# Kernel optimization log

Measured on AMD Instinct MI355X. Metric: run time of the kernel, lower is better.

## Reference

```python
import jax, jax.numpy as jnp
import numpy as np

N_E = 4096      # n_embed
E_DIM = 64      # embed_dim
BETA = 0.25
DECAY = 0.99
EPS = 1e-05


def setup_inputs() -> dict:
    key = jax.random.key(0)
    k1, k2, k3, k4 = jax.random.split(key, 4)
    z = jax.random.normal(k1, (4, 64, 16, 32, 32), dtype=jnp.float32)
    # codebook initialized uniform(-1/n_e, 1/n_e) as in the torch module
    embed_w = jax.random.uniform(k2, (N_E, E_DIM), dtype=jnp.float32,
                                 minval=-1.0 / N_E, maxval=1.0 / N_E)
    cluster_size = jax.random.uniform(k3, (N_E,), dtype=jnp.float32)
    embed_avg = jax.random.normal(k4, (N_E, E_DIM), dtype=jnp.float32) * 0.01
    return {"z": z, "embed_w": embed_w, "cluster_size": cluster_size,
            "embed_avg": embed_avg}


def reference(z, embed_w, cluster_size, embed_avg):
    sg = jax.lax.stop_gradient
    # b c d h w -> b d h w c
    zp = jnp.transpose(z, (0, 2, 3, 4, 1))
    zf = zp.reshape(-1, E_DIM)                      # [N, e_dim]
    n_tok = zf.shape[0]
    # squared L2 distances to every code: [N, n_e]
    d = ((zf * zf).sum(axis=1, keepdims=True)
         + (embed_w * embed_w).sum(axis=1)
         - 2.0 * jnp.einsum('bd,nd->bn', zf, embed_w))
    idx = jnp.argmin(d, axis=1)                     # [N]
    z_q = embed_w[idx].reshape(zp.shape)            # codebook gather
    # perplexity from code-usage histogram (== mean of one-hot encodings)
    counts = jnp.zeros((N_E,), zf.dtype).at[idx].add(1.0)
    avg_probs = counts / n_tok
    perplexity = jnp.exp(-jnp.sum(avg_probs * jnp.log(avg_probs + 1e-10)))
    # EMA buffer updates (training mode; pure buffer math, no gradient flow)
    embed_sum = jnp.zeros((N_E, E_DIM), zf.dtype).at[idx].add(sg(zf))  # one_hot.T @ zf
    new_cs = cluster_size * DECAY + (1.0 - DECAY) * counts
    new_ea = embed_avg * DECAY + (1.0 - DECAY) * embed_sum
    n = new_cs.sum()
    smoothed_cs = (new_cs + EPS) / (n + N_E * EPS) * n
    new_embed = new_ea / smoothed_cs[:, None]
    # commitment loss and straight-through estimator
    loss = BETA * jnp.mean((sg(z_q) - zp) ** 2)
    z_q_st = zp + sg(z_q - zp)
    out = jnp.transpose(z_q_st, (0, 4, 1, 2, 3))    # b d h w c -> b c d h w
    return (out, loss, perplexity, idx, new_embed, new_cs, new_ea)
```

## Files before the change

### kernel.cpp

```cpp
#include <hip/hip_runtime.h>

static constexpr int NE   = 4096;
static constexpr int ED   = 64;
static constexpr int NTOK = 65536;
static constexpr int NCHUNK = 8;
static constexpr int CPC  = NE / NCHUNK;

static constexpr long O_OUT  = 0;
static constexpr long O_LOSS = 4194304;
static constexpr long O_PERP = 4194305;
static constexpr long O_IDX  = 4194306;
static constexpr long O_NEMB = 4259842;
static constexpr long O_NCS  = 4521986;
static constexpr long O_NEA  = 4526082;

static constexpr size_t W_ACC   = 0;
static constexpr size_t W_CNT   = 32;
static constexpr size_t W_CUR   = 16416;
static constexpr size_t W_OFF   = 32800;
static constexpr size_t W_BSQ   = 49184;
static constexpr size_t W_IDX   = 65568;
static constexpr size_t W_BKT   = 327712;
static constexpr size_t W_LOSSP = 589856;
static constexpr size_t W_PKD   = 720928;
static constexpr size_t W_ZERO_BYTES = 32800;
static constexpr size_t W_PKD_BYTES  = 524288;

__global__ __launch_bounds__(256) void kBsq(const float* __restrict__ e,
                                            float* __restrict__ bsq) {
    int n = blockIdx.x * 256 + threadIdx.x;
    const float* er = e + (n << 6);
    float a0 = 0.f, a1 = 0.f, a2 = 0.f, a3 = 0.f;
#pragma unroll
    for (int k = 0; k < ED; k += 4) {
        a0 = fmaf(er[k+0], er[k+0], a0);
        a1 = fmaf(er[k+1], er[k+1], a1);
        a2 = fmaf(er[k+2], er[k+2], a2);
        a3 = fmaf(er[k+3], er[k+3], a3);
    }
    bsq[n] = (a0 + a1) + (a2 + a3);
}

__global__ __launch_bounds__(256, 2) void kArgmin(const float* __restrict__ z,
                                                  const float* __restrict__ e,
                                                  const float* __restrict__ bsq,
                                                  unsigned long long* __restrict__ packed) {
    int bid = blockIdx.x;
    int tb = bid >> 3;
    int chunk = bid & 7;
    int t = tb * 256 + threadIdx.x;
    int b = t >> 14;
    int s = t & 16383;
    const float* zp = z + (long)b * 1048576 + s;

    float zr[ED];
#pragma unroll
    for (int k = 0; k < ED; ++k) zr[k] = zp[k * 16384];
#pragma unroll
    for (int k = 0; k < ED; ++k) asm volatile("" : "+v"(zr[k]));

    float a0 = 0.f, a1 = 0.f, a2 = 0.f, a3 = 0.f;
#pragma unroll
    for (int k = 0; k < ED; k += 4) {
        a0 = fmaf(zr[k+0], zr[k+0], a0);
        a1 = fmaf(zr[k+1], zr[k+1], a1);
        a2 = fmaf(zr[k+2], zr[k+2], a2);
        a3 = fmaf(zr[k+3], zr[k+3], a3);
    }
    float A = (a0 + a1) + (a2 + a3);

    float best = __builtin_inff();
    int bidx = 0;
    int c0 = chunk << 9;
    for (int n = c0; n < c0 + CPC; ++n) {
        int nu = __builtin_amdgcn_readfirstlane(n);
        const float* __restrict__ er = e + (nu << 6);
        float bq = bsq[nu];
        float d0 = 0.f, d1 = 0.f, d2 = 0.f, d3 = 0.f;
#pragma unroll
        for (int k = 0; k < ED; k += 4) {
            d0 = fmaf(zr[k+0], er[k+0], d0);
            d1 = fmaf(zr[k+1], er[k+1], d1);
            d2 = fmaf(zr[k+2], er[k+2], d2);
            d3 = fmaf(zr[k+3], er[k+3], d3);
        }
        float dot = (d0 + d1) + (d2 + d3);
        float d = (A + bq) - 2.0f * dot;
        if (d < best) { best = d; bidx = n; }
    }
    unsigned long long pk =
        ((unsigned long long)__float_as_uint(best) << 32) | (unsigned)bidx;
    atomicMin(&packed[t], pk);
}

__global__ __launch_bounds__(256) void kFinish(const unsigned long long* __restrict__ packed,
                                               float* __restrict__ outIdxF,
                                               int* __restrict__ wsIdx,
                                               unsigned* __restrict__ counts) {
    int t = blockIdx.x * 256 + threadIdx.x;
    int idx = (int)(unsigned)(packed[t] & 0xFFFFFFFFull);
    outIdxF[t] = (float)idx;
    wsIdx[t]   = idx;
    atomicAdd(&counts[idx], 1u);
}

__global__ __launch_bounds__(256) void kOffsets(const unsigned* __restrict__ counts,
                                                unsigned* __restrict__ offsets) {
    __shared__ unsigned psum[256];
    int tid = threadIdx.x;
    unsigned local[16];
    unsigned s = 0;
#pragma unroll
    for (int j = 0; j < 16; ++j) { local[j] = s; s += counts[tid * 16 + j]; }
    psum[tid] = s;
    __syncthreads();
    unsigned base = 0;
    for (int i = 0; i < tid; ++i) base += psum[i];
#pragma unroll
    for (int j = 0; j < 16; ++j) offsets[tid * 16 + j] = base + local[j];
}

__global__ __launch_bounds__(256) void kScatter(const int* __restrict__ wsIdx,
                                                const unsigned* __restrict__ offsets,
                                                unsigned* __restrict__ cursor,
                                                int* __restrict__ bucket) {
    int t = blockIdx.x * 256 + threadIdx.x;
    int idx = wsIdx[t];
    unsigned pos = atomicAdd(&cursor[idx], 1u);
    bucket[offsets[idx] + pos] = t;
}

__global__ __launch_bounds__(256) void kEpilogue(const float* __restrict__ z,
                                                 const float* __restrict__ e,
                                                 const int* __restrict__ wsIdx,
                                                 float* __restrict__ out,
                                                 double* __restrict__ lossPart) {
    __shared__ double lp[4];
    long g = (long)blockIdx.x * 256 + threadIdx.x;
    int b = (int)(g >> 20);
    int r = (int)(g & 1048575);
    int k = r >> 14;
    int s = r & 16383;
    int t = (b << 14) | s;

    float zv = z[g];
    int n = wsIdx[t];
    float eq = e[(n << 6) + k];
    float diff = eq - zv;
    out[g] = zv + diff;

    double sq = (double)diff * (double)diff;
#pragma unroll
    for (int o = 32; o > 0; o >>= 1) sq += __shfl_down(sq, o);
    if ((threadIdx.x & 63) == 0) lp[threadIdx.x >> 6] = sq;
    __syncthreads();
    if (threadIdx.x == 0) lossPart[blockIdx.x] = (lp[0] + lp[1]) + (lp[2] + lp[3]);
}

__global__ __launch_bounds__(256) void kLoss(const double* __restrict__ lossPart,
                                             double* __restrict__ acc) {
    __shared__ double lp[4];
    double s = 0.0;
    for (int j = 0; j < 64; ++j) s += lossPart[threadIdx.x + j * 256];
#pragma unroll
    for (int o = 32; o > 0; o >>= 1) s += __shfl_down(s, o);
    if ((threadIdx.x & 63) == 0) lp[threadIdx.x >> 6] = s;
    __syncthreads();
    if (threadIdx.x == 0) acc[0] = (lp[0] + lp[1]) + (lp[2] + lp[3]);
}

__global__ __launch_bounds__(256) void kEma1(const float* __restrict__ cs,
                                             const unsigned* __restrict__ counts,
                                             float* __restrict__ outNcs,
                                             double* __restrict__ acc) {
    int n = blockIdx.x * 256 + threadIdx.x;
    float cf = (float)counts[n];
    float p1 = cs[n] * 0.99f;
    float p2 = 0.01f * cf;
    float ncs = p1 + p2;
    outNcs[n] = ncs;
    float p = cf * (1.0f / 65536.0f);
    float term = p * logf(p + 1e-10f);
    double dn = (double)ncs, dt = (double)term;
#pragma unroll
    for (int o = 32; o > 0; o >>= 1) { dn += __shfl_down(dn, o); dt += __shfl_down(dt, o); }
    if ((threadIdx.x & 63) == 0) {
        atomicAdd(&acc[1], dn);
        atomicAdd(&acc[2], dt);
    }
}

__global__ __launch_bounds__(64) void kEsumEma2(const float* __restrict__ z,
                                                const float* __restrict__ ea,
                                                const int* __restrict__ bucket,
                                                const unsigned* __restrict__ offsets,
                                                const unsigned* __restrict__ counts,
                                                const float* __restrict__ ncsArr,
                                                const double* __restrict__ acc,
                                                float* __restrict__ outNemb,
                                                float* __restrict__ outNea,
                                                float* __restrict__ outLoss,
                                                float* __restrict__ outPerp) {
    int n = blockIdx.x;
    int k = threadIdx.x;
    unsigned off = offsets[n];
    unsigned cnt = counts[n];
    float es = 0.f;
    for (unsigned i = 0; i < cnt; ++i) {
        int t = bucket[off + i];
        int b = t >> 14;
        int s = t & 16383;
        es += z[(long)b * 1048576 + k * 16384 + s];
    }
    float nea = ea[(n << 6) + k] * 0.99f + 0.01f * es;
    outNea[(n << 6) + k] = nea;
    float nt = (float)acc[1];
    float ncs = ncsArr[n];
    float sc = ((ncs + 1e-5f) / (nt + 0.04096f)) * nt;
    outNemb[(n << 6) + k] = nea / sc;
    if (n == 0 && k == 0) {
        double m = acc[0] / 4194304.0;
        outLoss[0] = 0.25f * (float)m;
        outPerp[0] = (float)exp(-acc[2]);
    }
}

extern "C" void kernel_launch(void* const* d_in, const int* in_sizes, int n_in,
                              void* d_out, int out_size, void* d_ws, size_t ws_size,
                              hipStream_t stream) {
    const float* z  = (const float*)d_in[0];
    const float* ew = (const float*)d_in[1];
    const float* cs = (const float*)d_in[2];
    const float* ea = (const float*)d_in[3];
    float* out = (float*)d_out;
    char* ws = (char*)d_ws;

    double*   acc    = (double*)(ws + W_ACC);
    unsigned* counts = (unsigned*)(ws + W_CNT);
    unsigned* cursor = (unsigned*)(ws + W_CUR);
    unsigned* offs   = (unsigned*)(ws + W_OFF);
    float*    bsq    = (float*)(ws + W_BSQ);
    int*      wsIdx  = (int*)(ws + W_IDX);
    int*      bucket = (int*)(ws + W_BKT);
    double*   lossP  = (double*)(ws + W_LOSSP);
    unsigned long long* packed = (unsigned long long*)(ws + W_PKD);

    hipMemsetAsync(ws, 0, W_ZERO_BYTES, stream);
    hipMemsetAsync(ws + W_PKD, 0xFF, W_PKD_BYTES, stream);
    kBsq<<<NE / 256, 256, 0, stream>>>(ew, bsq);
    kArgmin<<<(NTOK / 256) * NCHUNK, 256, 0, stream>>>(z, ew, bsq, packed);
    kFinish<<<NTOK / 256, 256, 0, stream>>>(packed, out + O_IDX, wsIdx, counts);
    kOffsets<<<1, 256, 0, stream>>>(counts, offs);
    kScatter<<<NTOK / 256, 256, 0, stream>>>(wsIdx, offs, cursor, bucket);
    kEpilogue<<<16384, 256, 0, stream>>>(z, ew, wsIdx, out + O_OUT, lossP);
    kLoss<<<1, 256, 0, stream>>>(lossP, acc);
    kEma1<<<NE / 256, 256, 0, stream>>>(cs, counts, out + O_NCS, acc);
    kEsumEma2<<<NE, 64, 0, stream>>>(z, ea, bucket, offs, counts, out + O_NCS, acc,
                                     out + O_NEMB, out + O_NEA,
                                     out + O_LOSS, out + O_PERP);
}
```

Before: 545.0 us.

## Rewrite argmin in inline asm with LDS-staged codebook and two tokens per thread

The codebook plus its squared norms is packed into an augmented 68-float row layout, and each block stages a 128-code chunk into LDS. A hand-written assembly loop has each thread hold two tokens' 64-dim vectors in registers and reuse every LDS-read code row for both tokens. The code space is split into 32 chunks instead of 8. The aim is to replace per-thread scalar/global codebook reads with wide LDS reads and to double arithmetic per load. The cost is heavy register pinning (about 238 VGPRs), fragile inline asm, and more atomicMin traffic from the extra chunks.

```diff
diff --git a/kernel.cpp b/kernel.cpp
--- a/kernel.cpp
+++ b/kernel.cpp
@@ -3,8 +3,11 @@
 static constexpr int NE   = 4096;
 static constexpr int ED   = 64;
 static constexpr int NTOK = 65536;
-static constexpr int NCHUNK = 8;
+static constexpr int NCHUNK = 32;
 static constexpr int CPC  = NE / NCHUNK;
+
+typedef float  f32x2 __attribute__((ext_vector_type(2)));
+typedef float  f32x4 __attribute__((ext_vector_type(4)));
 
 static constexpr long O_OUT  = 0;
 static constexpr long O_LOSS = 4194304;
@@ -18,18 +21,19 @@
 static constexpr size_t W_CNT   = 32;
 static constexpr size_t W_CUR   = 16416;
 static constexpr size_t W_OFF   = 32800;
-static constexpr size_t W_BSQ   = 49184;
-static constexpr size_t W_IDX   = 65568;
-static constexpr size_t W_BKT   = 327712;
-static constexpr size_t W_LOSSP = 589856;
-static constexpr size_t W_PKD   = 720928;
+static constexpr size_t W_IDX   = 49184;
+static constexpr size_t W_BKT   = 311328;
+static constexpr size_t W_LOSSP = 573472;
+static constexpr size_t W_PKD   = 704544;
+static constexpr size_t W_AUG   = 1228832;
 static constexpr size_t W_ZERO_BYTES = 32800;
 static constexpr size_t W_PKD_BYTES  = 524288;
 
-__global__ __launch_bounds__(256) void kBsq(const float* __restrict__ e,
-                                            float* __restrict__ bsq) {
+__global__ __launch_bounds__(256) void kAug(const float* __restrict__ e,
+                                            float* __restrict__ aug) {
     int n = blockIdx.x * 256 + threadIdx.x;
     const float* er = e + (n << 6);
+    float* row = aug + (long)n * 68;
     float a0 = 0.f, a1 = 0.f, a2 = 0.f, a3 = 0.f;
 #pragma unroll
     for (int k = 0; k < ED; k += 4) {
@@ -38,59 +42,209 @@
         a2 = fmaf(er[k+2], er[k+2], a2);
         a3 = fmaf(er[k+3], er[k+3], a3);
     }
-    bsq[n] = (a0 + a1) + (a2 + a3);
-}
+#pragma unroll
+    for (int k = 0; k < 16; ++k)
+        ((f32x4*)row)[k] = ((const f32x4*)er)[k];
+    row[64] = (a0 + a1) + (a2 + a3);
+}
+
+#define ZLD(VD) \
+    "global_load_dword v" #VD ", v233, %[zb]\n\t" \
+    "v_add_u32 v233, 0x10000, v233\n\t"
+#define AMUL(C, Z) "v_mul_f32 v" #C ", v" #Z ", v" #Z "\n\t"
+#define AFMA(C, Z) "v_fma_f32 v" #C ", v" #Z ", v" #Z ", v" #C "\n\t"
+#define AQ4(Z0,Z1,Z2,Z3) AFMA(225,Z0) AFMA(226,Z1) AFMA(227,Z2) AFMA(228,Z3)
+#define BQ4(Z0,Z1,Z2,Z3) AFMA(229,Z0) AFMA(230,Z1) AFMA(231,Z2) AFMA(232,Z3)
+#define M2(CA,CB,ZA,ZB,E) \
+    "v_mul_f32 v" #CA ", v" #ZA ", v" #E "\n\t" \
+    "v_mul_f32 v" #CB ", v" #ZB ", v" #E "\n\t"
+#define D2(CA,CB,ZA,ZB,E) \
+    "v_fma_f32 v" #CA ", v" #ZA ", v" #E ", v" #CA "\n\t" \
+    "v_fma_f32 v" #CB ", v" #ZB ", v" #E ", v" #CB "\n\t"
 
 __global__ __launch_bounds__(256, 2) void kArgmin(const float* __restrict__ z,
-                                                  const float* __restrict__ e,
-                                                  const float* __restrict__ bsq,
+                                                  const float* __restrict__ aug,
                                                   unsigned long long* __restrict__ packed) {
+    __shared__ alignas(16) float lds[CPC * 68 + 16];
     int bid = blockIdx.x;
-    int tb = bid >> 3;
-    int chunk = bid & 7;
-    int t = tb * 256 + threadIdx.x;
-    int b = t >> 14;
-    int s = t & 16383;
-    const float* zp = z + (long)b * 1048576 + s;
-
-    float zr[ED];
-#pragma unroll
-    for (int k = 0; k < ED; ++k) zr[k] = zp[k * 16384];
-#pragma unroll
-    for (int k = 0; k < ED; ++k) asm volatile("" : "+v"(zr[k]));
-
-    float a0 = 0.f, a1 = 0.f, a2 = 0.f, a3 = 0.f;
-#pragma unroll
-    for (int k = 0; k < ED; k += 4) {
-        a0 = fmaf(zr[k+0], zr[k+0], a0);
-        a1 = fmaf(zr[k+1], zr[k+1], a1);
-        a2 = fmaf(zr[k+2], zr[k+2], a2);
-        a3 = fmaf(zr[k+3], zr[k+3], a3);
+    int tb = bid >> 5;
+    int chunk = bid & 31;
+
+    {
+        const f32x2* src = (const f32x2*)(aug + (long)(chunk * CPC) * 68);
+        f32x2* dst = (f32x2*)lds;
+#pragma unroll
+        for (int i = 0; i < 17; ++i)
+            dst[threadIdx.x + i * 256] = src[threadIdx.x + i * 256];
     }
-    float A = (a0 + a1) + (a2 + a3);
-
-    float best = __builtin_inff();
-    int bidx = 0;
-    int c0 = chunk << 9;
-    for (int n = c0; n < c0 + CPC; ++n) {
-        int nu = __builtin_amdgcn_readfirstlane(n);
-        const float* __restrict__ er = e + (nu << 6);
-        float bq = bsq[nu];
-        float d0 = 0.f, d1 = 0.f, d2 = 0.f, d3 = 0.f;
-#pragma unroll
-        for (int k = 0; k < ED; k += 4) {
-            d0 = fmaf(zr[k+0], er[k+0], d0);
-            d1 = fmaf(zr[k+1], er[k+1], d1);
-            d2 = fmaf(zr[k+2], er[k+2], d2);
-            d3 = fmaf(zr[k+3], er[k+3], d3);
-        }
-        float dot = (d0 + d1) + (d2 + d3);
-        float d = (A + bq) - 2.0f * dot;
-        if (d < best) { best = d; bidx = n; }
-    }
-    unsigned long long pk =
-        ((unsigned long long)__float_as_uint(best) << 32) | (unsigned)bidx;
-    atomicMin(&packed[t], pk);
+    __syncthreads();
+
+    int t0 = tb * 512 + threadIdx.x;
+    int t1 = t0 + 256;
+    int b  = t0 >> 14;
+    int s0 = t0 & 16383;
+    unsigned off0 = ((unsigned)b * 1048576u + (unsigned)s0) * 4u;
+    unsigned off1 = off0 + 1024u;
+
+    int c0i = chunk * CPC;
+    float best0 = __builtin_inff(), best1 = __builtin_inff();
+    int bidx0 = c0i, bidx1 = c0i;
+    unsigned va0 = (unsigned)(unsigned long long)(&lds[0]);
+
+    asm volatile(
+        "v_mov_b32 v233, %[off0]\n\t"
+        ZLD(64)  ZLD(65)  ZLD(66)  ZLD(67)  ZLD(68)  ZLD(69)  ZLD(70)  ZLD(71)
+        ZLD(72)  ZLD(73)  ZLD(74)  ZLD(75)  ZLD(76)  ZLD(77)  ZLD(78)  ZLD(79)
+        ZLD(80)  ZLD(81)  ZLD(82)  ZLD(83)  ZLD(84)  ZLD(85)  ZLD(86)  ZLD(87)
+        ZLD(88)  ZLD(89)  ZLD(90)  ZLD(91)  ZLD(92)  ZLD(93)  ZLD(94)  ZLD(95)
+        ZLD(96)  ZLD(97)  ZLD(98)  ZLD(99)  ZLD(100) ZLD(101) ZLD(102) ZLD(103)
+        ZLD(104) ZLD(105) ZLD(106) ZLD(107) ZLD(108) ZLD(109) ZLD(110) ZLD(111)
+        ZLD(112) ZLD(113) ZLD(114) ZLD(115) ZLD(116) ZLD(117) ZLD(118) ZLD(119)
+        ZLD(120) ZLD(121) ZLD(122) ZLD(123) ZLD(124) ZLD(125) ZLD(126) ZLD(127)
+        "v_mov_b32 v233, %[off1]\n\t"
+        ZLD(128) ZLD(129) ZLD(130) ZLD(131) ZLD(132) ZLD(133) ZLD(134) ZLD(135)
+        ZLD(136) ZLD(137) ZLD(138) ZLD(139) ZLD(140) ZLD(141) ZLD(142) ZLD(143)
+        ZLD(144) ZLD(145) ZLD(146) ZLD(147) ZLD(148) ZLD(149) ZLD(150) ZLD(151)
+        ZLD(152) ZLD(153) ZLD(154) ZLD(155) ZLD(156) ZLD(157) ZLD(158) ZLD(159)
+        ZLD(160) ZLD(161) ZLD(162) ZLD(163) ZLD(164) ZLD(165) ZLD(166) ZLD(167)
+        ZLD(168) ZLD(169) ZLD(170) ZLD(171) ZLD(172) ZLD(173) ZLD(174) ZLD(175)
+        ZLD(176) ZLD(177) ZLD(178) ZLD(179) ZLD(180) ZLD(181) ZLD(182) ZLD(183)
+        ZLD(184) ZLD(185) ZLD(186) ZLD(187) ZLD(188) ZLD(189) ZLD(190) ZLD(191)
+        "s_waitcnt vmcnt(0)\n\t"
+        AMUL(225,64) AMUL(226,65) AMUL(227,66) AMUL(228,67)
+        AQ4(68,69,70,71)    AQ4(72,73,74,75)    AQ4(76,77,78,79)
+        AQ4(80,81,82,83)    AQ4(84,85,86,87)    AQ4(88,89,90,91)
+        AQ4(92,93,94,95)    AQ4(96,97,98,99)    AQ4(100,101,102,103)
+        AQ4(104,105,106,107) AQ4(108,109,110,111) AQ4(112,113,114,115)
+        AQ4(116,117,118,119) AQ4(120,121,122,123) AQ4(124,125,126,127)
+        "v_add_f32 v234, v225, v226\n\t"
+        "v_add_f32 v233, v227, v228\n\t"
+        "v_add_f32 v234, v234, v233\n\t"
+        AMUL(229,128) AMUL(230,129) AMUL(231,130) AMUL(232,131)
+        BQ4(132,133,134,135) BQ4(136,137,138,139) BQ4(140,141,142,143)
+        BQ4(144,145,146,147) BQ4(148,149,150,151) BQ4(152,153,154,155)
+        BQ4(156,157,158,159) BQ4(160,161,162,163) BQ4(164,165,166,167)
+        BQ4(168,169,170,171) BQ4(172,173,174,175) BQ4(176,177,178,179)
+        BQ4(180,181,182,183) BQ4(184,185,186,187) BQ4(188,189,190,191)
+        "v_add_f32 v235, v229, v230\n\t"
+        "v_add_f32 v233, v231, v232\n\t"
+        "v_add_f32 v235, v235, v233\n\t"
+        "s_mov_b32 s32, 0\n\t"
+        "v_mov_b32 v237, %[n0]\n\t"
+        "ds_read_b128 v[192:195], %[va] offset:0\n\t"
+        "ds_read_b128 v[196:199], %[va] offset:16\n\t"
+        "ds_read_b128 v[200:203], %[va] offset:32\n\t"
+        "ds_read_b128 v[204:207], %[va] offset:48\n\t"
+        "1:\n\t"
+        "ds_read_b128 v[208:211], %[va] offset:64\n\t"
+        "ds_read_b128 v[212:215], %[va] offset:80\n\t"
+        "ds_read_b128 v[216:219], %[va] offset:96\n\t"
+        "ds_read_b128 v[220:223], %[va] offset:112\n\t"
+        "s_waitcnt lgkmcnt(4)\n\t"
+        M2(225,229,64,128,192) M2(226,230,65,129,193)
+        M2(227,231,66,130,194) M2(228,232,67,131,195)
+        D2(225,229,68,132,196) D2(226,230,69,133,197)
+        D2(227,231,70,134,198) D2(228,232,71,135,199)
+        D2(225,229,72,136,200) D2(226,230,73,137,201)
+        D2(227,231,74,138,202) D2(228,232,75,139,203)
+        D2(225,229,76,140,204) D2(226,230,77,141,205)
+        D2(227,231,78,142,206) D2(228,232,79,143,207)
+        "ds_read_b128 v[192:195], %[va] offset:128\n\t"
+        "ds_read_b128 v[196:199], %[va] offset:144\n\t"
+        "ds_read_b128 v[200:203], %[va] offset:160\n\t"
+        "ds_read_b128 v[204:207], %[va] offset:176\n\t"
+        "s_waitcnt lgkmcnt(4)\n\t"
+        D2(225,229,80,144,208) D2(226,230,81,145,209)
+        D2(227,231,82,146,210) D2(228,232,83,147,211)
+        D2(225,229,84,148,212) D2(226,230,85,149,213)
+        D2(227,231,86,150,214) D2(228,232,87,151,215)
+        D2(225,229,88,152,216) D2(226,230,89,153,217)
+        D2(227,231,90,154,218) D2(228,232,91,155,219)
+        D2(225,229,92,156,220) D2(226,230,93,157,221)
+        D2(227,231,94,158,222) D2(228,232,95,159,223)
+        "ds_read_b128 v[208:211], %[va] offset:192\n\t"
+        "ds_read_b128 v[212:215], %[va] offset:208\n\t"
+        "ds_read_b128 v[216:219], %[va] offset:224\n\t"
+        "ds_read_b128 v[220:223], %[va] offset:240\n\t"
+        "ds_read_b32 v224, %[va] offset:256\n\t"
+        "s_waitcnt lgkmcnt(5)\n\t"
+        D2(225,229,96,160,192)  D2(226,230,97,161,193)
+        D2(227,231,98,162,194)  D2(228,232,99,163,195)
+        D2(225,229,100,164,196) D2(226,230,101,165,197)
+        D2(227,231,102,166,198) D2(228,232,103,167,199)
+        D2(225,229,104,168,200) D2(226,230,105,169,201)
+        D2(227,231,106,170,202) D2(228,232,107,171,203)
+        D2(225,229,108,172,204) D2(226,230,109,173,205)
+        D2(227,231,110,174,206) D2(228,232,111,175,207)
+        "v_add_u32 %[va], 0x110, %[va]\n\t"
+        "ds_read_b128 v[192:195], %[va] offset:0\n\t"
+        "ds_read_b128 v[196:199], %[va] offset:16\n\t"
+        "ds_read_b128 v[200:203], %[va] offset:32\n\t"
+        "ds_read_b128 v[204:207], %[va] offset:48\n\t"
+        "s_waitcnt lgkmcnt(4)\n\t"
+        D2(225,229,112,176,208) D2(226,230,113,177,209)
+        D2(227,231,114,178,210) D2(228,232,115,179,211)
+        D2(225,229,116,180,212) D2(226,230,117,181,213)
+        D2(227,231,118,182,214) D2(228,232,119,183,215)
+        D2(225,229,120,184,216) D2(226,230,121,185,217)
+        D2(227,231,122,186,218) D2(228,232,123,187,219)
+        D2(225,229,124,188,220) D2(226,230,125,189,221)
+        D2(227,231,126,190,222) D2(228,232,127,191,223)
+        "v_add_f32 v233, v225, v226\n\t"
+        "v_add_f32 v236, v227, v228\n\t"
+        "v_add_f32 v233, v233, v236\n\t"
+        "v_add_f32 v236, v224, v234\n\t"
+        "v_fma_f32 v233, -2.0, v233, v236\n\t"
+        "v_cmp_lt_f32 vcc, v233, %[best0]\n\t"
+        "v_cndmask_b32 %[best0], %[best0], v233, vcc\n\t"
+        "v_cndmask_b32 %[bidx0], %[bidx0], v237, vcc\n\t"
+        "v_add_f32 v233, v229, v230\n\t"
+        "v_add_f32 v236, v231, v232\n\t"
+        "v_add_f32 v233, v233, v236\n\t"
+        "v_add_f32 v236, v224, v235\n\t"
+        "v_fma_f32 v233, -2.0, v233, v236\n\t"
+        "v_cmp_lt_f32 vcc, v233, %[best1]\n\t"
+        "v_cndmask_b32 %[best1], %[best1], v233, vcc\n\t"
+        "v_cndmask_b32 %[bidx1], %[bidx1], v237, vcc\n\t"
+        "v_add_u32 v237, 1, v237\n\t"
+        "s_add_u32 s32, s32, 1\n\t"
+        "s_cmp_lt_u32 s32, 0x80\n\t"
+        "s_cbranch_scc1 1b\n\t"
+        "s_waitcnt lgkmcnt(0)\n\t"
+        : [best0]"+v"(best0), [bidx0]"+v"(bidx0),
+          [best1]"+v"(best1), [bidx1]"+v"(bidx1), [va]"+v"(va0)
+        : [zb]"s"(z), [off0]"v"(off0), [off1]"v"(off1), [n0]"v"(c0i)
+        : "s32",
+          "v64","v65","v66","v67","v68","v69","v70","v71",
+          "v72","v73","v74","v75","v76","v77","v78","v79",
+          "v80","v81","v82","v83","v84","v85","v86","v87",
+          "v88","v89","v90","v91","v92","v93","v94","v95",
+          "v96","v97","v98","v99","v100","v101","v102","v103",
+          "v104","v105","v106","v107","v108","v109","v110","v111",
+          "v112","v113","v114","v115","v116","v117","v118","v119",
+          "v120","v121","v122","v123","v124","v125","v126","v127",
+          "v128","v129","v130","v131","v132","v133","v134","v135",
+          "v136","v137","v138","v139","v140","v141","v142","v143",
+          "v144","v145","v146","v147","v148","v149","v150","v151",
+          "v152","v153","v154","v155","v156","v157","v158","v159",
+          "v160","v161","v162","v163","v164","v165","v166","v167",
+          "v168","v169","v170","v171","v172","v173","v174","v175",
+          "v176","v177","v178","v179","v180","v181","v182","v183",
+          "v184","v185","v186","v187","v188","v189","v190","v191",
+          "v192","v193","v194","v195","v196","v197","v198","v199",
+          "v200","v201","v202","v203","v204","v205","v206","v207",
+          "v208","v209","v210","v211","v212","v213","v214","v215",
+          "v216","v217","v218","v219","v220","v221","v222","v223",
+          "v224","v225","v226","v227","v228","v229","v230","v231",
+          "v232","v233","v234","v235","v236","v237",
+          "vcc","scc","memory");
+
+    unsigned long long pk0 =
+        ((unsigned long long)__float_as_uint(best0) << 32) | (unsigned)bidx0;
+    unsigned long long pk1 =
+        ((unsigned long long)__float_as_uint(best1) << 32) | (unsigned)bidx1;
+    atomicMin(&packed[t0], pk0);
+    atomicMin(&packed[t1], pk1);
 }
 
 __global__ __launch_bounds__(256) void kFinish(const unsigned long long* __restrict__ packed,
@@ -239,16 +393,16 @@
     unsigned* counts = (unsigned*)(ws + W_CNT);
     unsigned* cursor = (unsigned*)(ws + W_CUR);
     unsigned* offs   = (unsigned*)(ws + W_OFF);
-    float*    bsq    = (float*)(ws + W_BSQ);
     int*      wsIdx  = (int*)(ws + W_IDX);
     int*      bucket = (int*)(ws + W_BKT);
     double*   lossP  = (double*)(ws + W_LOSSP);
     unsigned long long* packed = (unsigned long long*)(ws + W_PKD);
+    float*    aug    = (float*)(ws + W_AUG);
 
     hipMemsetAsync(ws, 0, W_ZERO_BYTES, stream);
     hipMemsetAsync(ws + W_PKD, 0xFF, W_PKD_BYTES, stream);
-    kBsq<<<NE / 256, 256, 0, stream>>>(ew, bsq);
-    kArgmin<<<(NTOK / 256) * NCHUNK, 256, 0, stream>>>(z, ew, bsq, packed);
+    kAug<<<NE / 256, 256, 0, stream>>>(ew, aug);
+    kArgmin<<<(NTOK / 512) * NCHUNK, 256, 0, stream>>>(z, aug, packed);
     kFinish<<<NTOK / 256, 256, 0, stream>>>(packed, out + O_IDX, wsIdx, counts);
     kOffsets<<<1, 256, 0, stream>>>(counts, offs);
     kScatter<<<NTOK / 256, 256, 0, stream>>>(wsIdx, offs, cursor, bucket);
```

Result: slower. 576.1 us (+5.7%).

## Hand-write argmin inner loop in asm with two tokens per thread and scalar codebook prefetch

Applied to the files above, without the earlier changes.

The argmin kernel is rewritten as inline assembly. Each thread now handles two tokens, so every codebook scalar load is used for two dot products. Codebook rows are repacked into an augmented 68-float layout that carries the row's squared norm, and are streamed through SGPRs with s_load_dwordx16, prefetching the next row while the current one is computed. Occupancy is raised to 3 waves. The hard-coded VGPR/SGPR clobbers add register pressure and fragility, and tie-breaking order must match the reference.

```diff
diff --git a/kernel.cpp b/kernel.cpp
--- a/kernel.cpp
+++ b/kernel.cpp
@@ -5,6 +5,8 @@
 static constexpr int NTOK = 65536;
 static constexpr int NCHUNK = 8;
 static constexpr int CPC  = NE / NCHUNK;
+
+typedef float  f32x4 __attribute__((ext_vector_type(4)));
 
 static constexpr long O_OUT  = 0;
 static constexpr long O_LOSS = 4194304;
@@ -18,18 +20,19 @@
 static constexpr size_t W_CNT   = 32;
 static constexpr size_t W_CUR   = 16416;
 static constexpr size_t W_OFF   = 32800;
-static constexpr size_t W_BSQ   = 49184;
-static constexpr size_t W_IDX   = 65568;
-static constexpr size_t W_BKT   = 327712;
-static constexpr size_t W_LOSSP = 589856;
-static constexpr size_t W_PKD   = 720928;
+static constexpr size_t W_IDX   = 49184;
+static constexpr size_t W_BKT   = 311328;
+static constexpr size_t W_LOSSP = 573472;
+static constexpr size_t W_PKD   = 704544;
+static constexpr size_t W_AUG   = 1228832;
 static constexpr size_t W_ZERO_BYTES = 32800;
 static constexpr size_t W_PKD_BYTES  = 524288;
 
-__global__ __launch_bounds__(256) void kBsq(const float* __restrict__ e,
-                                            float* __restrict__ bsq) {
+__global__ __launch_bounds__(256) void kAug(const float* __restrict__ e,
+                                            float* __restrict__ aug) {
     int n = blockIdx.x * 256 + threadIdx.x;
     const float* er = e + (n << 6);
+    float* row = aug + (long)n * 68;
     float a0 = 0.f, a1 = 0.f, a2 = 0.f, a3 = 0.f;
 #pragma unroll
     for (int k = 0; k < ED; k += 4) {
@@ -38,59 +41,191 @@
         a2 = fmaf(er[k+2], er[k+2], a2);
         a3 = fmaf(er[k+3], er[k+3], a3);
     }
-    bsq[n] = (a0 + a1) + (a2 + a3);
-}
-
-__global__ __launch_bounds__(256, 2) void kArgmin(const float* __restrict__ z,
-                                                  const float* __restrict__ e,
-                                                  const float* __restrict__ bsq,
+#pragma unroll
+    for (int k = 0; k < 16; ++k)
+        ((f32x4*)row)[k] = ((const f32x4*)er)[k];
+    row[64] = (a0 + a1) + (a2 + a3);
+}
+
+#define ZLD(VD) \
+    "global_load_dword v" #VD ", v162, %[zb]\n\t" \
+    "v_add_u32 v162, 0x10000, v162\n\t"
+#define AMUL(C, Z) "v_mul_f32 v" #C ", v" #Z ", v" #Z "\n\t"
+#define AFMA(C, Z) "v_fma_f32 v" #C ", v" #Z ", v" #Z ", v" #C "\n\t"
+#define AQ4(Z0,Z1,Z2,Z3) AFMA(152,Z0) AFMA(153,Z1) AFMA(154,Z2) AFMA(155,Z3)
+#define BQ4(Z0,Z1,Z2,Z3) AFMA(156,Z0) AFMA(157,Z1) AFMA(158,Z2) AFMA(159,Z3)
+#define MS2(CA,CB,ZA,ZB,SR) \
+    "v_mul_f32 v" #CA ", v" #ZA ", s" #SR "\n\t" \
+    "v_mul_f32 v" #CB ", v" #ZB ", s" #SR "\n\t"
+#define DS2(CA,CB,ZA,ZB,SR) \
+    "v_fma_f32 v" #CA ", v" #ZA ", s" #SR ", v" #CA "\n\t" \
+    "v_fma_f32 v" #CB ", v" #ZB ", s" #SR ", v" #CB "\n\t"
+
+__global__ __launch_bounds__(256, 3) void kArgmin(const float* __restrict__ z,
+                                                  const float* __restrict__ aug,
                                                   unsigned long long* __restrict__ packed) {
     int bid = blockIdx.x;
     int tb = bid >> 3;
     int chunk = bid & 7;
-    int t = tb * 256 + threadIdx.x;
-    int b = t >> 14;
-    int s = t & 16383;
-    const float* zp = z + (long)b * 1048576 + s;
-
-    float zr[ED];
-#pragma unroll
-    for (int k = 0; k < ED; ++k) zr[k] = zp[k * 16384];
-#pragma unroll
-    for (int k = 0; k < ED; ++k) asm volatile("" : "+v"(zr[k]));
-
-    float a0 = 0.f, a1 = 0.f, a2 = 0.f, a3 = 0.f;
-#pragma unroll
-    for (int k = 0; k < ED; k += 4) {
-        a0 = fmaf(zr[k+0], zr[k+0], a0);
-        a1 = fmaf(zr[k+1], zr[k+1], a1);
-        a2 = fmaf(zr[k+2], zr[k+2], a2);
-        a3 = fmaf(zr[k+3], zr[k+3], a3);
-    }
-    float A = (a0 + a1) + (a2 + a3);
-
-    float best = __builtin_inff();
-    int bidx = 0;
-    int c0 = chunk << 9;
-    for (int n = c0; n < c0 + CPC; ++n) {
-        int nu = __builtin_amdgcn_readfirstlane(n);
-        const float* __restrict__ er = e + (nu << 6);
-        float bq = bsq[nu];
-        float d0 = 0.f, d1 = 0.f, d2 = 0.f, d3 = 0.f;
-#pragma unroll
-        for (int k = 0; k < ED; k += 4) {
-            d0 = fmaf(zr[k+0], er[k+0], d0);
-            d1 = fmaf(zr[k+1], er[k+1], d1);
-            d2 = fmaf(zr[k+2], er[k+2], d2);
-            d3 = fmaf(zr[k+3], er[k+3], d3);
-        }
-        float dot = (d0 + d1) + (d2 + d3);
-        float d = (A + bq) - 2.0f * dot;
-        if (d < best) { best = d; bidx = n; }
-    }
-    unsigned long long pk =
-        ((unsigned long long)__float_as_uint(best) << 32) | (unsigned)bidx;
-    atomicMin(&packed[t], pk);
+
+    int t0 = tb * 512 + threadIdx.x;
+    int t1 = t0 + 256;
+    int b  = t0 >> 14;
+    int s0 = t0 & 16383;
+    unsigned off0 = ((unsigned)b * 1048576u + (unsigned)s0) * 4u;
+    unsigned off1 = off0 + 1024u;
+
+    int c0i = chunk * CPC;
+    float best0 = __builtin_inff(), best1 = __builtin_inff();
+    int bidx0 = c0i, bidx1 = c0i;
+    const float* rowPtr = aug + (long)c0i * 68;
+
+    asm volatile(
+        "v_mov_b32 v162, %[off0]\n\t"
+        ZLD(24)  ZLD(25)  ZLD(26)  ZLD(27)  ZLD(28)  ZLD(29)  ZLD(30)  ZLD(31)
+        ZLD(32)  ZLD(33)  ZLD(34)  ZLD(35)  ZLD(36)  ZLD(37)  ZLD(38)  ZLD(39)
+        ZLD(40)  ZLD(41)  ZLD(42)  ZLD(43)  ZLD(44)  ZLD(45)  ZLD(46)  ZLD(47)
+        ZLD(48)  ZLD(49)  ZLD(50)  ZLD(51)  ZLD(52)  ZLD(53)  ZLD(54)  ZLD(55)
+        ZLD(56)  ZLD(57)  ZLD(58)  ZLD(59)  ZLD(60)  ZLD(61)  ZLD(62)  ZLD(63)
+        ZLD(64)  ZLD(65)  ZLD(66)  ZLD(67)  ZLD(68)  ZLD(69)  ZLD(70)  ZLD(71)
+        ZLD(72)  ZLD(73)  ZLD(74)  ZLD(75)  ZLD(76)  ZLD(77)  ZLD(78)  ZLD(79)
+        ZLD(80)  ZLD(81)  ZLD(82)  ZLD(83)  ZLD(84)  ZLD(85)  ZLD(86)  ZLD(87)
+        "v_mov_b32 v162, %[off1]\n\t"
+        ZLD(88)  ZLD(89)  ZLD(90)  ZLD(91)  ZLD(92)  ZLD(93)  ZLD(94)  ZLD(95)
+        ZLD(96)  ZLD(97)  ZLD(98)  ZLD(99)  ZLD(100) ZLD(101) ZLD(102) ZLD(103)
+        ZLD(104) ZLD(105) ZLD(106) ZLD(107) ZLD(108) ZLD(109) ZLD(110) ZLD(111)
+        ZLD(112) ZLD(113) ZLD(114) ZLD(115) ZLD(116) ZLD(117) ZLD(118) ZLD(119)
+        ZLD(120) ZLD(121) ZLD(122) ZLD(123) ZLD(124) ZLD(125) ZLD(126) ZLD(127)
+        ZLD(128) ZLD(129) ZLD(130) ZLD(131) ZLD(132) ZLD(133) ZLD(134) ZLD(135)
+        ZLD(136) ZLD(137) ZLD(138) ZLD(139) ZLD(140) ZLD(141) ZLD(142) ZLD(143)
+        ZLD(144) ZLD(145) ZLD(146) ZLD(147) ZLD(148) ZLD(149) ZLD(150) ZLD(151)
+        "s_waitcnt vmcnt(0)\n\t"
+        AMUL(152,24) AMUL(153,25) AMUL(154,26) AMUL(155,27)
+        AQ4(28,29,30,31)  AQ4(32,33,34,35)  AQ4(36,37,38,39)
+        AQ4(40,41,42,43)  AQ4(44,45,46,47)  AQ4(48,49,50,51)
+        AQ4(52,53,54,55)  AQ4(56,57,58,59)  AQ4(60,61,62,63)
+        AQ4(64,65,66,67)  AQ4(68,69,70,71)  AQ4(72,73,74,75)
+        AQ4(76,77,78,79)  AQ4(80,81,82,83)  AQ4(84,85,86,87)
+        "v_add_f32 v160, v152, v153\n\t"
+        "v_add_f32 v161, v154, v155\n\t"
+        "v_add_f32 v160, v160, v161\n\t"
+        AMUL(156,88) AMUL(157,89) AMUL(158,90) AMUL(159,91)
+        BQ4(92,93,94,95)     BQ4(96,97,98,99)     BQ4(100,101,102,103)
+        BQ4(104,105,106,107) BQ4(108,109,110,111) BQ4(112,113,114,115)
+        BQ4(116,117,118,119) BQ4(120,121,122,123) BQ4(124,125,126,127)
+        BQ4(128,129,130,131) BQ4(132,133,134,135) BQ4(136,137,138,139)
+        BQ4(140,141,142,143) BQ4(144,145,146,147) BQ4(148,149,150,151)
+        "v_add_f32 v161, v156, v157\n\t"
+        "v_add_f32 v152, v158, v159\n\t"
+        "v_add_f32 v161, v161, v152\n\t"
+        "s_mov_b64 s[34:35], %[ap]\n\t"
+        "s_mov_b32 s33, 0\n\t"
+        "v_mov_b32 v162, %[n0]\n\t"
+        "s_load_dwordx16 s[36:51], s[34:35], 0x0\n\t"
+        "s_load_dwordx16 s[52:67], s[34:35], 0x40\n\t"
+        "1:\n\t"
+        "s_waitcnt lgkmcnt(0)\n\t"
+        "s_load_dwordx16 s[68:83], s[34:35], 0x80\n\t"
+        "s_load_dwordx16 s[84:99], s[34:35], 0xc0\n\t"
+        "s_load_dword s100, s[34:35], 0x100\n\t"
+        MS2(152,156,24,88,36) MS2(153,157,25,89,37)
+        MS2(154,158,26,90,38) MS2(155,159,27,91,39)
+        DS2(152,156,28,92,40) DS2(153,157,29,93,41)
+        DS2(154,158,30,94,42) DS2(155,159,31,95,43)
+        DS2(152,156,32,96,44) DS2(153,157,33,97,45)
+        DS2(154,158,34,98,46) DS2(155,159,35,99,47)
+        DS2(152,156,36,100,48) DS2(153,157,37,101,49)
+        DS2(154,158,38,102,50) DS2(155,159,39,103,51)
+        DS2(152,156,40,104,52) DS2(153,157,41,105,53)
+        DS2(154,158,42,106,54) DS2(155,159,43,107,55)
+        DS2(152,156,44,108,56) DS2(153,157,45,109,57)
+        DS2(154,158,46,110,58) DS2(155,159,47,111,59)
+        DS2(152,156,48,112,60) DS2(153,157,49,113,61)
+        DS2(154,158,50,114,62) DS2(155,159,51,115,63)
+        DS2(152,156,52,116,64) DS2(153,157,53,117,65)
+        DS2(154,158,54,118,66) DS2(155,159,55,119,67)
+        "s_waitcnt lgkmcnt(0)\n\t"
+        "s_add_u32 s34, s34, 272\n\t"
+        "s_addc_u32 s35, s35, 0\n\t"
+        "s_load_dwordx16 s[36:51], s[34:35], 0x0\n\t"
+        "s_load_dwordx16 s[52:67], s[34:35], 0x40\n\t"
+        DS2(152,156,56,120,68) DS2(153,157,57,121,69)
+        DS2(154,158,58,122,70) DS2(155,159,59,123,71)
+        DS2(152,156,60,124,72) DS2(153,157,61,125,73)
+        DS2(154,158,62,126,74) DS2(155,159,63,127,75)
+        DS2(152,156,64,128,76) DS2(153,157,65,129,77)
+        DS2(154,158,66,130,78) DS2(155,159,67,131,79)
+        DS2(152,156,68,132,80) DS2(153,157,69,133,81)
+        DS2(154,158,70,134,82) DS2(155,159,71,135,83)
+        DS2(152,156,72,136,84) DS2(153,157,73,137,85)
+        DS2(154,158,74,138,86) DS2(155,159,75,139,87)
+        DS2(152,156,76,140,88) DS2(153,157,77,141,89)
+        DS2(154,158,78,142,90) DS2(155,159,79,143,91)
+        DS2(152,156,80,144,92) DS2(153,157,81,145,93)
+        DS2(154,158,82,146,94) DS2(155,159,83,147,95)
+        DS2(152,156,84,148,96) DS2(153,157,85,149,97)
+        DS2(154,158,86,150,98) DS2(155,159,87,151,99)
+        "v_add_f32 v152, v152, v153\n\t"
+        "v_add_f32 v154, v154, v155\n\t"
+        "v_add_f32 v152, v152, v154\n\t"
+        "v_add_f32 v153, s100, v160\n\t"
+        "v_fma_f32 v152, -2.0, v152, v153\n\t"
+        "v_cmp_lt_f32 vcc, v152, %[best0]\n\t"
+        "v_cndmask_b32 %[best0], %[best0], v152, vcc\n\t"
+        "v_cndmask_b32 %[bidx0], %[bidx0], v162, vcc\n\t"
+        "v_add_f32 v156, v156, v157\n\t"
+        "v_add_f32 v158, v158, v159\n\t"
+        "v_add_f32 v156, v156, v158\n\t"
+        "v_add_f32 v157, s100, v161\n\t"
+        "v_fma_f32 v156, -2.0, v156, v157\n\t"
+        "v_cmp_lt_f32 vcc, v156, %[best1]\n\t"
+        "v_cndmask_b32 %[best1], %[best1], v156, vcc\n\t"
+        "v_cndmask_b32 %[bidx1], %[bidx1], v162, vcc\n\t"
+        "v_add_u32 v162, 1, v162\n\t"
+        "s_add_u32 s33, s33, 1\n\t"
+        "s_cmp_lt_u32 s33, 0x200\n\t"
+        "s_cbranch_scc1 1b\n\t"
+        "s_waitcnt lgkmcnt(0)\n\t"
+        : [best0]"+v"(best0), [bidx0]"+v"(bidx0),
+          [best1]"+v"(best1), [bidx1]"+v"(bidx1)
+        : [zb]"s"(z), [ap]"s"(rowPtr),
+          [off0]"v"(off0), [off1]"v"(off1), [n0]"v"(c0i)
+        : "s33","s34","s35",
+          "s36","s37","s38","s39","s40","s41","s42","s43",
+          "s44","s45","s46","s47","s48","s49","s50","s51",
+          "s52","s53","s54","s55","s56","s57","s58","s59",
+          "s60","s61","s62","s63","s64","s65","s66","s67",
+          "s68","s69","s70","s71","s72","s73","s74","s75",
+          "s76","s77","s78","s79","s80","s81","s82","s83",
+          "s84","s85","s86","s87","s88","s89","s90","s91",
+          "s92","s93","s94","s95","s96","s97","s98","s99",
+          "s100",
+          "v24","v25","v26","v27","v28","v29","v30","v31",
+          "v32","v33","v34","v35","v36","v37","v38","v39",
+          "v40","v41","v42","v43","v44","v45","v46","v47",
+          "v48","v49","v50","v51","v52","v53","v54","v55",
+          "v56","v57","v58","v59","v60","v61","v62","v63",
+          "v64","v65","v66","v67","v68","v69","v70","v71",
+          "v72","v73","v74","v75","v76","v77","v78","v79",
+          "v80","v81","v82","v83","v84","v85","v86","v87",
+          "v88","v89","v90","v91","v92","v93","v94","v95",
+          "v96","v97","v98","v99","v100","v101","v102","v103",
+          "v104","v105","v106","v107","v108","v109","v110","v111",
+          "v112","v113","v114","v115","v116","v117","v118","v119",
+          "v120","v121","v122","v123","v124","v125","v126","v127",
+          "v128","v129","v130","v131","v132","v133","v134","v135",
+          "v136","v137","v138","v139","v140","v141","v142","v143",
+          "v144","v145","v146","v147","v148","v149","v150","v151",
+          "v152","v153","v154","v155","v156","v157","v158","v159",
+          "v160","v161","v162",
+          "vcc","scc","memory");
+
+    unsigned long long pk0 =
+        ((unsigned long long)__float_as_uint(best0) << 32) | (unsigned)bidx0;
+    unsigned long long pk1 =
+        ((unsigned long long)__float_as_uint(best1) << 32) | (unsigned)bidx1;
+    atomicMin(&packed[t0], pk0);
+    atomicMin(&packed[t1], pk1);
 }
 
 __global__ __launch_bounds__(256) void kFinish(const unsigned long long* __restrict__ packed,
@@ -239,16 +374,16 @@
     unsigned* counts = (unsigned*)(ws + W_CNT);
     unsigned* cursor = (unsigned*)(ws + W_CUR);
     unsigned* offs   = (unsigned*)(ws + W_OFF);
-    float*    bsq    = (float*)(ws + W_BSQ);
     int*      wsIdx  = (int*)(ws + W_IDX);
     int*      bucket = (int*)(ws + W_BKT);
     double*   lossP  = (double*)(ws + W_LOSSP);
     unsigned long long* packed = (unsigned long long*)(ws + W_PKD);
+    float*    aug    = (float*)(ws + W_AUG);
 
     hipMemsetAsync(ws, 0, W_ZERO_BYTES, stream);
     hipMemsetAsync(ws + W_PKD, 0xFF, W_PKD_BYTES, stream);
-    kBsq<<<NE / 256, 256, 0, stream>>>(ew, bsq);
-    kArgmin<<<(NTOK / 256) * NCHUNK, 256, 0, stream>>>(z, ew, bsq, packed);
+    kAug<<<NE / 256, 256, 0, stream>>>(ew, aug);
+    kArgmin<<<(NTOK / 512) * NCHUNK, 256, 0, stream>>>(z, aug, packed);
     kFinish<<<NTOK / 256, 256, 0, stream>>>(packed, out + O_IDX, wsIdx, counts);
     kOffsets<<<1, 256, 0, stream>>>(counts, offs);
     kScatter<<<NTOK / 256, 256, 0, stream>>>(wsIdx, offs, cursor, bucket);
```

Result: slower. 641.5 us (+17.7%).
